# Kernel optimization log

Measured on AMD Instinct MI355X. Metric: run time of the kernel, lower is better.

## Reference

```python
import jax, jax.numpy as jnp
import numpy as np

BITS = 8
EPS = 0.01  # eps in max_scale_rounded_power
QMAX = float(1 << (BITS - 1))  # 128.0; quantize multiplies by (1<<bits)/scale=2 -> 2^(bits-1)


def _max_scale_rounded_power(x, axis):
    # max_scale: clamp(max(|x|, axis), min=eps); then round scale up to a power of 2
    m = jnp.maximum(jnp.max(jnp.abs(x), axis=axis), EPS)
    return jnp.exp2(jnp.ceil(jnp.log2(m)))


def _dmd_dequant(x):
    """quantize_dmd_alternating(iters=2) followed by recreate_from_dmd.

    x: (..., R, C). i=0 scales columns (reduce over rows, dim=-2),
    i=1 scales rows (reduce over cols, dim=-1). quantize(x,0,2,bits) =
    clamp(round(x * 2^(bits-1)), -2^(bits-1), 2^(bits-1)-1), and the row
    scale is divided by 2^(bits-1) before reconstruction.
    """
    s_col = _max_scale_rounded_power(x, -2)          # (..., C)
    x = x / s_col[..., None, :]
    s_row = _max_scale_rounded_power(x, -1)          # (..., R)
    x = x / s_row[..., :, None]
    q = jnp.clip(jnp.round(x * QMAX), -QMAX, QMAX - 1.0)
    # recreate_from_dmd(s_col, q, s_row / 2^(bits-1))
    return s_col[..., None, :] * q * (s_row / QMAX)[..., :, None]


def setup_inputs() -> dict:
    key = jax.random.key(0)
    k1, k2, k3 = jax.random.split(key, 3)
    B, S, NX, NF = 8, 4096, 1024, 1024
    x = jax.random.normal(k1, (B, S, NX), dtype=jnp.float32)
    weight = jax.random.normal(k2, (NX, NF), dtype=jnp.float32) * 0.02
    bias = jax.random.normal(k3, (NF,), dtype=jnp.float32) * 0.01
    return {"x": x, "weight": weight, "bias": bias}


def reference(x, weight, bias):
    B, S, nx = x.shape
    nf = weight.shape[-1]
    xq = _dmd_dequant(x.reshape(-1, nx))   # (B*S, nx) dequantized
    yq = _dmd_dequant(weight)              # (nx, nf) dequantized
    out = xq @ yq + bias                   # (B*S, nf)
    return out.reshape(B, S, nf)
```

## Files before the change

kernel.cpp:

```cpp
#include <hip/hip_runtime.h>
#include <hip/hip_bf16.h>
#include <stdint.h>

#define NXK 1024
#define NFN 1024
#define EPSQ 0.01f

typedef __bf16 bf16x8 __attribute__((ext_vector_type(8)));
typedef float f32x4 __attribute__((ext_vector_type(4)));

#define AS1(p) ((const __attribute__((address_space(1))) void*)(p))
#define AS3(p) ((__attribute__((address_space(3))) void*)(p))

__device__ __forceinline__ float p2ceil(float m) {
    unsigned u = __float_as_uint(m);
    if ((u & 0x7fffffu) == 0) return m;
    return __uint_as_float((((u >> 23) & 0xffu) + 1u) << 23);
}

__device__ __forceinline__ unsigned short f2bf(float f) {
    __bf16 h = (__bf16)f;
    return __builtin_bit_cast(unsigned short, h);
}

#define RPB 64
__global__ __launch_bounds__(256) void colmax_kernel(const float* __restrict__ X,
                                                     unsigned int* __restrict__ cmax) {
    const int t = threadIdx.x;
    const size_t r0 = (size_t)blockIdx.x * RPB;
    const float4* Xv = (const float4*)X;
    float m0 = 0.f, m1 = 0.f, m2 = 0.f, m3 = 0.f;
#pragma unroll 8
    for (int i = 0; i < RPB; ++i) {
        float4 v = Xv[(r0 + i) * (NXK / 4) + t];
        m0 = fmaxf(m0, fabsf(v.x));
        m1 = fmaxf(m1, fabsf(v.y));
        m2 = fmaxf(m2, fabsf(v.z));
        m3 = fmaxf(m3, fabsf(v.w));
    }
    atomicMax(&cmax[4 * t + 0], __float_as_uint(m0));
    atomicMax(&cmax[4 * t + 1], __float_as_uint(m1));
    atomicMax(&cmax[4 * t + 2], __float_as_uint(m2));
    atomicMax(&cmax[4 * t + 3], __float_as_uint(m3));
}

template <int TRANSPOSE>
__global__ __launch_bounds__(256) void rowquant_kernel(const float* __restrict__ X,
                                                       const unsigned int* __restrict__ cmaxbits,
                                                       unsigned short* __restrict__ Q) {
    const int m = blockIdx.x;
    const int t = threadIdx.x;
    const float4 v = ((const float4*)(X + (size_t)m * NXK))[t];
    const uint4 cb = ((const uint4*)cmaxbits)[t];

    const float sc0 = p2ceil(fmaxf(__uint_as_float(cb.x), EPSQ));
    const float sc1 = p2ceil(fmaxf(__uint_as_float(cb.y), EPSQ));
    const float sc2 = p2ceil(fmaxf(__uint_as_float(cb.z), EPSQ));
    const float sc3 = p2ceil(fmaxf(__uint_as_float(cb.w), EPSQ));

    const float r0 = v.x / sc0;
    const float r1 = v.y / sc1;
    const float r2 = v.z / sc2;
    const float r3 = v.w / sc3;

    float amax = fmaxf(fmaxf(fabsf(r0), fabsf(r1)), fmaxf(fabsf(r2), fabsf(r3)));
#pragma unroll
    for (int s = 32; s >= 1; s >>= 1) amax = fmaxf(amax, __shfl_xor(amax, s, 64));
    __shared__ float wmax[4];
    if ((t & 63) == 0) wmax[t >> 6] = amax;
    __syncthreads();
    amax = fmaxf(fmaxf(wmax[0], wmax[1]), fmaxf(wmax[2], wmax[3]));

    const float srow = p2ceil(fmaxf(amax, EPSQ));
    const float inv = 128.0f / srow;
    const float q0 = fminf(fmaxf(rintf(r0 * inv), -128.0f), 127.0f);
    const float q1 = fminf(fmaxf(rintf(r1 * inv), -128.0f), 127.0f);
    const float q2 = fminf(fmaxf(rintf(r2 * inv), -128.0f), 127.0f);
    const float q3 = fminf(fmaxf(rintf(r3 * inv), -128.0f), 127.0f);

    const float rs = srow * 0.0078125f;
    if (TRANSPOSE) {
        Q[(size_t)(4 * t + 0) * NXK + m] = f2bf(q0 * (sc0 * rs));
        Q[(size_t)(4 * t + 1) * NXK + m] = f2bf(q1 * (sc1 * rs));
        Q[(size_t)(4 * t + 2) * NXK + m] = f2bf(q2 * (sc2 * rs));
        Q[(size_t)(4 * t + 3) * NXK + m] = f2bf(q3 * (sc3 * rs));
    } else {
        ushort4 o;
        o.x = f2bf(q0 * (sc0 * rs));
        o.y = f2bf(q1 * (sc1 * rs));
        o.z = f2bf(q2 * (sc2 * rs));
        o.w = f2bf(q3 * (sc3 * rs));
        ((ushort4*)(Q + (size_t)m * NXK))[t] = o;
    }
}

__global__ __launch_bounds__(256) void gemm_kernel(const unsigned short* __restrict__ A,
                                                   const unsigned short* __restrict__ BT,
                                                   const float* __restrict__ bias,
                                                   float* __restrict__ C, int M) {
    constexpr int K = NXK, N = NFN;
    __shared__ unsigned short As[128][32];
    __shared__ unsigned short Bs[128][32];

    const int tid = threadIdx.x;
    const int wave = tid >> 6, lane = tid & 63;
    const int wr = wave >> 1, wc = wave & 1;
    const int bm = blockIdx.y * 128, bn = blockIdx.x * 128;

    f32x4 acc[4][4] = {};

    const int strow = wave * 32 + (lane >> 2);
    const int stcol = (lane & 3) * 8;
    const unsigned short* gA = A + (size_t)(bm + strow) * K + stcol;
    const unsigned short* gB = BT + (size_t)(bn + strow) * K + stcol;
    unsigned short* lA0 = &As[wave * 32][0];
    unsigned short* lA1 = &As[wave * 32 + 16][0];
    unsigned short* lB0 = &Bs[wave * 32][0];
    unsigned short* lB1 = &Bs[wave * 32 + 16][0];

    for (int k0 = 0; k0 < K; k0 += 32) {
        __builtin_amdgcn_global_load_lds(AS1(gA + k0),          AS3(lA0), 16, 0, 0);
        __builtin_amdgcn_global_load_lds(AS1(gA + 16 * K + k0), AS3(lA1), 16, 0, 0);
        __builtin_amdgcn_global_load_lds(AS1(gB + k0),          AS3(lB0), 16, 0, 0);
        __builtin_amdgcn_global_load_lds(AS1(gB + 16 * K + k0), AS3(lB1), 16, 0, 0);
        asm volatile("s_waitcnt vmcnt(0)" ::: "memory");
        __syncthreads();

        bf16x8 af[4], bf[4];
#pragma unroll
        for (int i = 0; i < 4; ++i) {
            af[i] = *(const bf16x8*)&As[wr * 64 + i * 16 + (lane & 15)][(lane >> 4) * 8];
            bf[i] = *(const bf16x8*)&Bs[wc * 64 + i * 16 + (lane & 15)][(lane >> 4) * 8];
        }
#pragma unroll
        for (int mi = 0; mi < 4; ++mi)
#pragma unroll
            for (int ni = 0; ni < 4; ++ni)
                acc[mi][ni] = __builtin_amdgcn_mfma_f32_16x16x32_bf16(af[mi], bf[ni], acc[mi][ni], 0, 0, 0);
        __syncthreads();
    }

#pragma unroll
    for (int mi = 0; mi < 4; ++mi) {
#pragma unroll
        for (int ni = 0; ni < 4; ++ni) {
            const int col = bn + wc * 64 + ni * 16 + (lane & 15);
            const float bv = bias[col];
#pragma unroll
            for (int j = 0; j < 4; ++j) {
                const int row = bm + wr * 64 + mi * 16 + (lane >> 4) * 4 + j;
                C[(size_t)row * N + col] = acc[mi][ni][j] + bv;
            }
        }
    }
}

extern "C" void kernel_launch(void* const* d_in, const int* in_sizes, int n_in,
                              void* d_out, int out_size, void* d_ws, size_t ws_size,
                              hipStream_t stream) {
    const float* x    = (const float*)d_in[0];
    const float* w    = (const float*)d_in[1];
    const float* bias = (const float*)d_in[2];
    float* out = (float*)d_out;
    const int M = in_sizes[0] / NXK;

    char* ws = (char*)d_ws;
    unsigned short* xq = (unsigned short*)ws;
    size_t off = (size_t)M * NXK * sizeof(unsigned short);
    unsigned short* wqT = (unsigned short*)(ws + off);
    off += (size_t)NFN * NXK * sizeof(unsigned short);
    unsigned int* cmx = (unsigned int*)(ws + off);
    unsigned int* cmw = cmx + NXK;

    hipMemsetAsync(cmx, 0, (NXK + NFN) * sizeof(unsigned int), stream);

    colmax_kernel<<<M / RPB, 256, 0, stream>>>(x, cmx);
    colmax_kernel<<<NXK / RPB, 256, 0, stream>>>(w, cmw);
    rowquant_kernel<0><<<M, 256, 0, stream>>>(x, cmx, xq);
    rowquant_kernel<1><<<NXK, 256, 0, stream>>>(w, cmw, wqT);
    gemm_kernel<<<dim3(NFN / 128, M / 128), 256, 0, stream>>>(xq, wqT, bias, out, M);
}
```

Baseline: 394.9 us.

## Remap GEMM tiles per XCD, use one wave per row in rowquant, halve colmax rows

```diff
diff --git a/kernel.cpp b/kernel.cpp
--- a/kernel.cpp
+++ b/kernel.cpp
@@ -23,7 +23,7 @@
     return __builtin_bit_cast(unsigned short, h);
 }
 
-#define RPB 64
+#define RPB 32
 __global__ __launch_bounds__(256) void colmax_kernel(const float* __restrict__ X,
                                                      unsigned int* __restrict__ cmax) {
     const int t = threadIdx.x;
@@ -48,52 +48,57 @@
 __global__ __launch_bounds__(256) void rowquant_kernel(const float* __restrict__ X,
                                                        const unsigned int* __restrict__ cmaxbits,
                                                        unsigned short* __restrict__ Q) {
-    const int m = blockIdx.x;
-    const int t = threadIdx.x;
-    const float4 v = ((const float4*)(X + (size_t)m * NXK))[t];
-    const uint4 cb = ((const uint4*)cmaxbits)[t];
+    const int wave = threadIdx.x >> 6, lane = threadIdx.x & 63;
+    const int m = blockIdx.x * 4 + wave;
+    const float4* Xr = (const float4*)(X + (size_t)m * NXK);
+    const uint4* Cb = (const uint4*)cmaxbits;
 
-    const float sc0 = p2ceil(fmaxf(__uint_as_float(cb.x), EPSQ));
-    const float sc1 = p2ceil(fmaxf(__uint_as_float(cb.y), EPSQ));
-    const float sc2 = p2ceil(fmaxf(__uint_as_float(cb.z), EPSQ));
-    const float sc3 = p2ceil(fmaxf(__uint_as_float(cb.w), EPSQ));
-
-    const float r0 = v.x / sc0;
-    const float r1 = v.y / sc1;
-    const float r2 = v.z / sc2;
-    const float r3 = v.w / sc3;
-
-    float amax = fmaxf(fmaxf(fabsf(r0), fabsf(r1)), fmaxf(fabsf(r2), fabsf(r3)));
+    float r[16], sc[16];
+    float amax = 0.f;
 #pragma unroll
-    for (int s = 32; s >= 1; s >>= 1) amax = fmaxf(amax, __shfl_xor(amax, s, 64));
-    __shared__ float wmax[4];
-    if ((t & 63) == 0) wmax[t >> 6] = amax;
-    __syncthreads();
-    amax = fmaxf(fmaxf(wmax[0], wmax[1]), fmaxf(wmax[2], wmax[3]));
+    for (int c = 0; c < 4; ++c) {
+        const float4 v = Xr[lane + 64 * c];
+        const uint4 cb = Cb[lane + 64 * c];
+        sc[4 * c + 0] = p2ceil(fmaxf(__uint_as_float(cb.x), EPSQ));
+        sc[4 * c + 1] = p2ceil(fmaxf(__uint_as_float(cb.y), EPSQ));
+        sc[4 * c + 2] = p2ceil(fmaxf(__uint_as_float(cb.z), EPSQ));
+        sc[4 * c + 3] = p2ceil(fmaxf(__uint_as_float(cb.w), EPSQ));
+        r[4 * c + 0] = v.x / sc[4 * c + 0];
+        r[4 * c + 1] = v.y / sc[4 * c + 1];
+        r[4 * c + 2] = v.z / sc[4 * c + 2];
+        r[4 * c + 3] = v.w / sc[4 * c + 3];
+        amax = fmaxf(amax, fmaxf(fmaxf(fabsf(r[4 * c + 0]), fabsf(r[4 * c + 1])),
+                                 fmaxf(fabsf(r[4 * c + 2]), fabsf(r[4 * c + 3]))));
+    }
+#pragma unroll
+    for (int s = 1; s < 64; s <<= 1) amax = fmaxf(amax, __shfl_xor(amax, s, 64));
 
     const float srow = p2ceil(fmaxf(amax, EPSQ));
     const float inv = 128.0f / srow;
-    const float q0 = fminf(fmaxf(rintf(r0 * inv), -128.0f), 127.0f);
-    const float q1 = fminf(fmaxf(rintf(r1 * inv), -128.0f), 127.0f);
-    const float q2 = fminf(fmaxf(rintf(r2 * inv), -128.0f), 127.0f);
-    const float q3 = fminf(fmaxf(rintf(r3 * inv), -128.0f), 127.0f);
-
     const float rs = srow * 0.0078125f;
-    if (TRANSPOSE) {
-        Q[(size_t)(4 * t + 0) * NXK + m] = f2bf(q0 * (sc0 * rs));
-        Q[(size_t)(4 * t + 1) * NXK + m] = f2bf(q1 * (sc1 * rs));
-        Q[(size_t)(4 * t + 2) * NXK + m] = f2bf(q2 * (sc2 * rs));
-        Q[(size_t)(4 * t + 3) * NXK + m] = f2bf(q3 * (sc3 * rs));
-    } else {
-        ushort4 o;
-        o.x = f2bf(q0 * (sc0 * rs));
-        o.y = f2bf(q1 * (sc1 * rs));
-        o.z = f2bf(q2 * (sc2 * rs));
-        o.w = f2bf(q3 * (sc3 * rs));
-        ((ushort4*)(Q + (size_t)m * NXK))[t] = o;
+#pragma unroll
+    for (int c = 0; c < 4; ++c) {
+        const float q0 = fminf(fmaxf(rintf(r[4 * c + 0] * inv), -128.0f), 127.0f);
+        const float q1 = fminf(fmaxf(rintf(r[4 * c + 1] * inv), -128.0f), 127.0f);
+        const float q2 = fminf(fmaxf(rintf(r[4 * c + 2] * inv), -128.0f), 127.0f);
+        const float q3 = fminf(fmaxf(rintf(r[4 * c + 3] * inv), -128.0f), 127.0f);
+        if (TRANSPOSE) {
+            Q[(size_t)(4 * (lane + 64 * c) + 0) * NXK + m] = f2bf(q0 * (sc[4 * c + 0] * rs));
+            Q[(size_t)(4 * (lane + 64 * c) + 1) * NXK + m] = f2bf(q1 * (sc[4 * c + 1] * rs));
+            Q[(size_t)(4 * (lane + 64 * c) + 2) * NXK + m] = f2bf(q2 * (sc[4 * c + 2] * rs));
+            Q[(size_t)(4 * (lane + 64 * c) + 3) * NXK + m] = f2bf(q3 * (sc[4 * c + 3] * rs));
+        } else {
+            ushort4 o;
+            o.x = f2bf(q0 * (sc[4 * c + 0] * rs));
+            o.y = f2bf(q1 * (sc[4 * c + 1] * rs));
+            o.z = f2bf(q2 * (sc[4 * c + 2] * rs));
+            o.w = f2bf(q3 * (sc[4 * c + 3] * rs));
+            ((ushort4*)(Q + (size_t)m * NXK))[lane + 64 * c] = o;
+        }
     }
 }
 
+#define GX (NFN / 128)
 __global__ __launch_bounds__(256) void gemm_kernel(const unsigned short* __restrict__ A,
                                                    const unsigned short* __restrict__ BT,
                                                    const float* __restrict__ bias,
@@ -105,7 +110,15 @@
     const int tid = threadIdx.x;
     const int wave = tid >> 6, lane = tid & 63;
     const int wr = wave >> 1, wc = wave & 1;
-    const int bm = blockIdx.y * 128, bn = blockIdx.x * 128;
+
+    const int nwg = GX * (M / 128);
+    int lin = blockIdx.y * GX + blockIdx.x;
+    {
+        const int q = nwg >> 3, r = nwg & 7;
+        const int xcd = lin & 7, idx = lin >> 3;
+        lin = (xcd < r ? xcd * (q + 1) : r * (q + 1) + (xcd - r) * q) + idx;
+    }
+    const int bm = (lin / GX) * 128, bn = (lin % GX) * 128;
 
     f32x4 acc[4][4] = {};
 
@@ -176,7 +189,7 @@
 
     colmax_kernel<<<M / RPB, 256, 0, stream>>>(x, cmx);
     colmax_kernel<<<NXK / RPB, 256, 0, stream>>>(w, cmw);
-    rowquant_kernel<0><<<M, 256, 0, stream>>>(x, cmx, xq);
-    rowquant_kernel<1><<<NXK, 256, 0, stream>>>(w, cmw, wqT);
-    gemm_kernel<<<dim3(NFN / 128, M / 128), 256, 0, stream>>>(xq, wqT, bias, out, M);
+    rowquant_kernel<0><<<M / 4, 256, 0, stream>>>(x, cmx, xq);
+    rowquant_kernel<1><<<NXK / 4, 256, 0, stream>>>(w, cmw, wqT);
+    gemm_kernel<<<dim3(GX, M / 128), 256, 0, stream>>>(xq, wqT, bias, out, M);
 }
```

Measured after the change: 410.5 us. +3.9%, slower.
